# Kernel optimization log

Hardware: AMD Instinct MI355X
Metric: run time of the kernel (lower is better)

## Reference

```python
import jax, jax.numpy as jnp
import numpy as np


def _topk_gate(v, k):
    # keep values >= k-th largest (ties kept, matching torch semantics)
    topk_vals = jax.lax.top_k(v, k)[0]          # (B, k)
    thr = topk_vals[:, -1:]                      # (B, 1)
    return v * (v >= thr).astype(v.dtype)


def setup_inputs() -> dict:
    key = jax.random.key(0)
    ks = jax.random.split(key, 12)
    B, S, D, R, M = 8, 2048, 1024, 64, 256
    H = 4 * D
    def lin(k, fan_out, fan_in):
        bound = 1.0 / np.sqrt(fan_in)
        return jax.random.uniform(k, (fan_out, fan_in), jnp.float32, -bound, bound)
    def bias(k, fan_out, fan_in):
        bound = 1.0 / np.sqrt(fan_in)
        return jax.random.uniform(k, (fan_out,), jnp.float32, -bound, bound)
    return {
        "x": jax.random.normal(ks[0], (B, S, D), jnp.float32),
        "state": jnp.zeros((B, M), jnp.float32),
        "U_w": lin(ks[1], R, D),
        "V_w": lin(ks[2], R, D),
        "w1": lin(ks[3], H, D),
        "b1": bias(ks[4], H, D),
        "w2": lin(ks[5], D, H),
        "b2": bias(ks[6], D, H),
        "win_w": lin(ks[7], M, D),
        "win_b": bias(ks[8], M, D),
        "wstate": lin(ks[9], M, M),
        "gamma": jnp.float32(0.9),
        "top_k": 32,
    }


def reference(x, state, U_w, V_w, w1, b1, w2, b2, win_w, win_b, wstate, gamma, top_k):
    # outputs depend only on x (residual + FFN), computed vectorized over seq.
    h = jax.nn.relu(jnp.einsum("bsd,hd->bsh", x, w1) + b1)
    outputs = x + jnp.einsum("bsh,dh->bsd", h, w2) + b2   # (B, S, D)
    # Note: U_proj / V_proj are computed but unused in the original forward
    # (dead code); omitted here as they do not affect outputs or memory.

    # precompute W_in projection for all timesteps: (B, S, M)
    x_proj = jnp.einsum("bsd,md->bsm", x, win_w) + win_b

    def step(carry, xp_t):
        st, mem = carry
        su = jax.nn.relu(st @ wstate.T + xp_t)            # (B, M)
        g = _topk_gate(su, top_k)
        mem = gamma * mem + (1.0 - gamma) * g
        return (g, mem), None

    (_, memory), _ = jax.lax.scan(step, (state, state), jnp.swapaxes(x_proj, 0, 1))
    return outputs, memory
```

## Files before the change

kernel.cpp:

```cpp
#include <hip/hip_runtime.h>
#include <stdint.h>

#define BB 8
#define SS 2048
#define DD 1024
#define HH 4096
#define MM 256

typedef short bf16x8 __attribute__((ext_vector_type(8)));
typedef float f32x4 __attribute__((ext_vector_type(4)));

__device__ inline unsigned short f2bf(float f){
  unsigned u = __builtin_bit_cast(unsigned, f);
  return (unsigned short)((u + 0x7FFFu + ((u >> 16) & 1u)) >> 16);
}

__global__ void ssma_pack_bf16(const float* __restrict__ src,
                               unsigned short* __restrict__ dst, int n4){
  int i = blockIdx.x * blockDim.x + threadIdx.x;
  if (i < n4){
    float4 v = ((const float4*)src)[i];
    ushort4 o;
    o.x = f2bf(v.x); o.y = f2bf(v.y); o.z = f2bf(v.z); o.w = f2bf(v.w);
    ((ushort4*)dst)[i] = o;
  }
}

template<int EPI>
__global__ __launch_bounds__(256) void ssma_gemm_bt(
    const unsigned short* __restrict__ A, const unsigned short* __restrict__ Bw,
    int K, int N, const float* __restrict__ bias,
    const float* __restrict__ resid, void* __restrict__ Cout)
{
  __shared__ uint4 As4[512];
  __shared__ uint4 Bs4[512];
  unsigned short* As = (unsigned short*)As4;
  unsigned short* Bs = (unsigned short*)Bs4;

  const int tid  = threadIdx.x;
  const int lane = tid & 63;
  const int wv   = tid >> 6;
  const int wm   = wv >> 1, wn = wv & 1;
  const int m0   = blockIdx.y * 128;
  const int n0   = blockIdx.x * 128;
  const int kq   = lane >> 4;
  const int rl   = lane & 15;

  f32x4 acc[4][4];
#pragma unroll
  for (int a = 0; a < 4; ++a)
#pragma unroll
    for (int b = 0; b < 4; ++b) acc[a][b] = (f32x4){0.f, 0.f, 0.f, 0.f};

  for (int k0 = 0; k0 < K; k0 += 32){
    __syncthreads();
#pragma unroll
    for (int i = 0; i < 2; ++i){
      int c  = tid + 256 * i;
      int r  = c >> 2;
      int c8 = (c & 3) * 8;
      As4[c] = *(const uint4*)(A  + (size_t)(m0 + r) * K + k0 + c8);
      Bs4[c] = *(const uint4*)(Bw + (size_t)(n0 + r) * K + k0 + c8);
    }
    __syncthreads();

    const bf16x8* Ap = (const bf16x8*)As;
    const bf16x8* Bp = (const bf16x8*)Bs;
    bf16x8 af[4], bfr[4];
#pragma unroll
    for (int mi = 0; mi < 4; ++mi) af[mi]  = Ap[(wm * 64 + mi * 16 + rl) * 4 + kq];
#pragma unroll
    for (int ni = 0; ni < 4; ++ni) bfr[ni] = Bp[(wn * 64 + ni * 16 + rl) * 4 + kq];
#pragma unroll
    for (int mi = 0; mi < 4; ++mi)
#pragma unroll
      for (int ni = 0; ni < 4; ++ni)
        acc[mi][ni] = __builtin_amdgcn_mfma_f32_16x16x32_bf16(af[mi], bfr[ni], acc[mi][ni], 0, 0, 0);
  }

#pragma unroll
  for (int mi = 0; mi < 4; ++mi){
#pragma unroll
    for (int ni = 0; ni < 4; ++ni){
      int col = n0 + wn * 64 + ni * 16 + rl;
      float bv = bias[col];
#pragma unroll
      for (int r = 0; r < 4; ++r){
        int row = m0 + wm * 64 + mi * 16 + kq * 4 + r;
        float v = acc[mi][ni][r] + bv;
        if (EPI == 0){
          v = fmaxf(v, 0.0f);
          ((unsigned short*)Cout)[(size_t)row * N + col] = f2bf(v);
        } else {
          v += resid[(size_t)row * N + col];
          ((float*)Cout)[(size_t)row * N + col] = v;
        }
      }
    }
  }
}

__global__ __launch_bounds__(256) void ssma_gemm3_f32(
    const float* __restrict__ A, const float* __restrict__ Bw,
    const float* __restrict__ bias, float* __restrict__ C)
{
  __shared__ float As[64][17];
  __shared__ float Bs[64][17];
  const int tid = threadIdx.x;
  const int tx = tid & 15, ty = tid >> 4;
  const int m0 = blockIdx.y * 64, n0 = blockIdx.x * 64;
  float acc[4][4];
#pragma unroll
  for (int i = 0; i < 4; ++i)
#pragma unroll
    for (int j = 0; j < 4; ++j) acc[i][j] = 0.f;

  for (int k0 = 0; k0 < DD; k0 += 16){
    __syncthreads();
#pragma unroll
    for (int i = 0; i < 4; ++i){
      int e = tid + 256 * i;
      int r = e >> 4, c = e & 15;
      As[r][c] = A [(size_t)(m0 + r) * DD + k0 + c];
      Bs[r][c] = Bw[(size_t)(n0 + r) * DD + k0 + c];
    }
    __syncthreads();
#pragma unroll
    for (int kk = 0; kk < 16; ++kk){
      float a[4], b[4];
#pragma unroll
      for (int i = 0; i < 4; ++i) a[i] = As[ty * 4 + i][kk];
#pragma unroll
      for (int j = 0; j < 4; ++j) b[j] = Bs[tx * 4 + j][kk];
#pragma unroll
      for (int i = 0; i < 4; ++i)
#pragma unroll
        for (int j = 0; j < 4; ++j) acc[i][j] = fmaf(a[i], b[j], acc[i][j]);
    }
  }
#pragma unroll
  for (int i = 0; i < 4; ++i){
    int row = m0 + ty * 4 + i;
#pragma unroll
    for (int j = 0; j < 4; ++j){
      int col = n0 + tx * 4 + j;
      C[(size_t)row * MM + col] = acc[i][j] + bias[col];
    }
  }
}

__global__ __launch_bounds__(256) void ssma_transpose(
    const float* __restrict__ A, float* __restrict__ At)
{
  __shared__ float t[32][33];
  const int tx = threadIdx.x & 31, ty = threadIdx.x >> 5;
  const int x0 = blockIdx.x * 32, y0 = blockIdx.y * 32;
#pragma unroll
  for (int r = 0; r < 32; r += 8)
    t[ty + r][tx] = A[(size_t)(y0 + ty + r) * MM + x0 + tx];
  __syncthreads();
#pragma unroll
  for (int r = 0; r < 32; r += 8)
    At[(size_t)(x0 + ty + r) * MM + y0 + tx] = t[tx][ty + r];
}

__global__ __launch_bounds__(512) void ssma_scan2(
    const float* __restrict__ xproj, const float* __restrict__ state,
    const float* __restrict__ wT, const float* __restrict__ gamma_p,
    const int* __restrict__ topk_p, float* __restrict__ mem_out)
{
  __shared__ __align__(16) float su_all[MM];
  __shared__ __align__(16) float su_pos[MM + 32];
  __shared__ __align__(16) float val_list[MM + 8];
  __shared__ __align__(16) int   idx_list[MM + 8];
  __shared__ unsigned long long  umask[4];
  __shared__ unsigned int        kmask[8];

  const int tid  = threadIdx.x;
  const int wv   = tid >> 6;
  const int lane = tid & 63;
  const int b    = blockIdx.x;
  const float gamma = *gamma_p;
  const float omg   = 1.0f - gamma;
  const int   rk    = *topk_p - 1;

  const int m  = tid;
  const int hl = lane & 31;
  const int h  = lane >> 5;
  const int m2 = wv * 32 + hl;

  const float* xp  = xproj + (size_t)b * SS * MM;
  const float* wTm = wT + m;

  float mem = state[b * MM + m2];

  int nk_ch;
  float st0 = 0.0f;
  if (wv < 4){
    st0 = state[b * MM + m];
    unsigned long long pmi = __ballot(st0 != 0.0f);
    if (lane == 0) umask[wv] = pmi;
  }
  __syncthreads();
  {
    unsigned long long u0 = umask[0], u1 = umask[1], u2 = umask[2], u3 = umask[3];
    int nk = __popcll(u0) + __popcll(u1) + __popcll(u2) + __popcll(u3);
    if (wv < 4 && st0 != 0.0f){
      int before = (wv > 0 ? __popcll(u0) : 0) + (wv > 1 ? __popcll(u1) : 0)
                 + (wv > 2 ? __popcll(u2) : 0);
      unsigned long long pmw = (wv == 0 ? u0 : wv == 1 ? u1 : wv == 2 ? u2 : u3);
      int pos = before + __popcll(pmw & ((1ull << lane) - 1ull));
      idx_list[pos] = m << 8;
      val_list[pos] = st0;
    }
    if (tid < 8){ idx_list[nk + tid] = 0; val_list[nk + tid] = 0.0f; }
    nk_ch = (nk + 7) >> 3;
  }
  __syncthreads();

  float xp_cur = (wv < 4) ? xp[m] : 0.0f;

  for (int t = 0; t < SS; ++t){
    float su = 0.0f;
    unsigned long long pm = 0;
    float xp_next = 0.0f;
    if (wv < 4){
      int tn = (t + 1 < SS) ? t + 1 : SS - 1;
      xp_next = xp[(size_t)tn * MM + m];
      float s0=0.f,s1=0.f,s2=0.f,s3=0.f,s4=0.f,s5=0.f,s6=0.f,s7=0.f;
      const int4*   ipb = (const int4*)idx_list;
      const float4* vpb = (const float4*)val_list;
      for (int c = 0; c < nk_ch; ++c){
        int4   ia = ipb[2*c], ib = ipb[2*c+1];
        float4 va = vpb[2*c], vb = vpb[2*c+1];
        float w0 = wTm[ia.x], w1 = wTm[ia.y], w2 = wTm[ia.z], w3 = wTm[ia.w];
        float w4 = wTm[ib.x], w5 = wTm[ib.y], w6 = wTm[ib.z], w7 = wTm[ib.w];
        s0 = fmaf(w0, va.x, s0); s1 = fmaf(w1, va.y, s1);
        s2 = fmaf(w2, va.z, s2); s3 = fmaf(w3, va.w, s3);
        s4 = fmaf(w4, vb.x, s4); s5 = fmaf(w5, vb.y, s5);
        s6 = fmaf(w6, vb.z, s6); s7 = fmaf(w7, vb.w, s7);
      }
      float s = ((s0 + s1) + (s2 + s3)) + ((s4 + s5) + (s6 + s7));
      su = fmaxf(s + xp_cur, 0.0f);
      su_all[m] = su;
      pm = __ballot(su > 0.0f);
      if (lane == 0) umask[wv] = pm;
    }
    __syncthreads();

    int P;
    {
      unsigned long long u0 = umask[0], u1 = umask[1], u2 = umask[2], u3 = umask[3];
      P = __popcll(u0) + __popcll(u1) + __popcll(u2) + __popcll(u3);
      if (wv < 4 && su > 0.0f){
        int before = (wv > 0 ? __popcll(u0) : 0) + (wv > 1 ? __popcll(u1) : 0)
                   + (wv > 2 ? __popcll(u2) : 0);
        int pos = before + __popcll(pm & ((1ull << lane) - 1ull));
        su_pos[pos] = su;
      }
    }
    if (tid < 32) su_pos[P + tid] = 0.0f;
    __syncthreads();

    float su2 = su_all[m2];
    int CH16 = ((P + 31) >> 5) << 1;
    int half = CH16 >> 1;
    int base4 = h * half * 4;
    int cnt = 0;
    const float4* spp = (const float4*)su_pos;
    for (int c = 0; c < half; ++c){
      float4 a = spp[base4 + 4*c + 0];
      float4 q = spp[base4 + 4*c + 1];
      float4 r = spp[base4 + 4*c + 2];
      float4 d = spp[base4 + 4*c + 3];
      cnt += (a.x > su2) + (a.y > su2) + (a.z > su2) + (a.w > su2)
           + (q.x > su2) + (q.y > su2) + (q.z > su2) + (q.w > su2)
           + (r.x > su2) + (r.y > su2) + (r.z > su2) + (r.w > su2)
           + (d.x > su2) + (d.y > su2) + (d.z > su2) + (d.w > su2);
    }
    cnt += __shfl_xor(cnt, 32);
    float g = (su2 > 0.0f && cnt <= rk) ? su2 : 0.0f;
    if (h == 0) mem = fmaf(gamma, mem, omg * g);
    unsigned int km = (unsigned int)(__ballot(h == 0 && g > 0.0f) & 0xffffffffull);
    if (lane == 0) kmask[wv] = km;
    __syncthreads();

    {
      int nk = 0, before2 = 0;
#pragma unroll
      for (int wi = 0; wi < 8; ++wi){
        int pc = __popc(kmask[wi]);
        nk += pc;
        if (wi < wv) before2 += pc;
      }
      if (h == 0 && g > 0.0f){
        int pos2 = before2 + __popc(km & ((1u << hl) - 1u));
        idx_list[pos2] = m2 << 8;
        val_list[pos2] = g;
      }
      if (tid < 8){ idx_list[nk + tid] = 0; val_list[nk + tid] = 0.0f; }
      nk_ch = (nk + 7) >> 3;
    }
    xp_cur = xp_next;
    __syncthreads();
  }
  if (h == 0) mem_out[b * MM + m2] = mem;
}

extern "C" void kernel_launch(void* const* d_in, const int* in_sizes, int n_in,
                              void* d_out, int out_size, void* d_ws, size_t ws_size,
                              hipStream_t stream)
{
  const float* x      = (const float*)d_in[0];
  const float* state  = (const float*)d_in[1];
  const float* w1     = (const float*)d_in[4];
  const float* b1     = (const float*)d_in[5];
  const float* w2     = (const float*)d_in[6];
  const float* b2     = (const float*)d_in[7];
  const float* win_w  = (const float*)d_in[8];
  const float* win_b  = (const float*)d_in[9];
  const float* wstate = (const float*)d_in[10];
  const float* gammap = (const float*)d_in[11];
  const int*   topkp  = (const int*)d_in[12];

  float* out  = (float*)d_out;
  float* memo = out + (size_t)BB * SS * DD;

  char* ws = (char*)d_ws;
  unsigned short* xb   = (unsigned short*)(ws);
  unsigned short* w1b  = (unsigned short*)(ws + 33554432);
  unsigned short* w2b  = (unsigned short*)(ws + 41943040);
  unsigned short* hbuf = (unsigned short*)(ws + 50331648);
  float*          xprj = (float*)(ws + 184549376);
  float*          wT   = (float*)(ws + 33554432);

  ssma_pack_bf16<<<16384, 256, 0, stream>>>(x,  xb,  4194304);
  ssma_pack_bf16<<<4096,  256, 0, stream>>>(w1, w1b, 1048576);
  ssma_pack_bf16<<<4096,  256, 0, stream>>>(w2, w2b, 1048576);

  ssma_gemm3_f32<<<dim3(4, 256), 256, 0, stream>>>(x, win_w, win_b, xprj);

  ssma_gemm_bt<0><<<dim3(32, 128), 256, 0, stream>>>(xb, w1b, 1024, 4096, b1, nullptr, (void*)hbuf);

  ssma_transpose<<<dim3(8, 8), 256, 0, stream>>>(wstate, wT);

  ssma_gemm_bt<1><<<dim3(8, 128), 256, 0, stream>>>(hbuf, w2b, 4096, 1024, b2, x, (void*)out);

  ssma_scan2<<<BB, 512, 0, stream>>>(xprj, state, wT, gammap, topkp, memo);
}
```

Before: 5.781 ms.

## Rework scan kernel to 1024 threads with 4-way rank counting and unrolled gather

The sequential top-k scan kernel now runs 1024 threads per batch row instead of 512. Each of the 256 state elements gets four threads for the rank count, cutting per-thread comparison work, and the results are combined with two shuffles. The sparse matvec fully unrolls the first 32 active entries, since top_k=32 makes that the common case, and pads the list to multiples of 16. The cost is more barrier participants per step, wider block-level synchronization, and an extra loop for larger active sets.

```diff
diff --git a/kernel.cpp b/kernel.cpp
--- a/kernel.cpp
+++ b/kernel.cpp
@@ -164,17 +164,17 @@
     At[(size_t)(x0 + ty + r) * MM + y0 + tx] = t[tx][ty + r];
 }
 
-__global__ __launch_bounds__(512) void ssma_scan2(
+__global__ __launch_bounds__(1024) void ssma_scan4(
     const float* __restrict__ xproj, const float* __restrict__ state,
     const float* __restrict__ wT, const float* __restrict__ gamma_p,
     const int* __restrict__ topk_p, float* __restrict__ mem_out)
 {
   __shared__ __align__(16) float su_all[MM];
   __shared__ __align__(16) float su_pos[MM + 32];
-  __shared__ __align__(16) float val_list[MM + 8];
-  __shared__ __align__(16) int   idx_list[MM + 8];
-  __shared__ unsigned long long  umask[4];
-  __shared__ unsigned int        kmask[8];
+  __shared__ __align__(16) int   kidx[MM + 32];
+  __shared__ __align__(16) float kval[MM + 32];
+  __shared__ __align__(16) unsigned long long umask[4];
+  __shared__ __align__(16) int   kmask16[16];
 
   const int tid  = threadIdx.x;
   const int wv   = tid >> 6;
@@ -184,127 +184,156 @@
   const float omg   = 1.0f - gamma;
   const int   rk    = *topk_p - 1;
 
-  const int m  = tid;
-  const int hl = lane & 31;
-  const int h  = lane >> 5;
-  const int m2 = wv * 32 + hl;
+  const int r = tid >> 2;
+  const int q = tid & 3;
 
   const float* xp  = xproj + (size_t)b * SS * MM;
-  const float* wTm = wT + m;
-
-  float mem = state[b * MM + m2];
-
-  int nk_ch;
+  const float* wTm = wT + tid;
+
+  float mem = state[b * MM + r];
+
   float st0 = 0.0f;
-  if (wv < 4){
-    st0 = state[b * MM + m];
+  if (tid < MM){
+    st0 = state[b * MM + tid];
     unsigned long long pmi = __ballot(st0 != 0.0f);
     if (lane == 0) umask[wv] = pmi;
   }
   __syncthreads();
+  int nkp;
   {
     unsigned long long u0 = umask[0], u1 = umask[1], u2 = umask[2], u3 = umask[3];
     int nk = __popcll(u0) + __popcll(u1) + __popcll(u2) + __popcll(u3);
-    if (wv < 4 && st0 != 0.0f){
+    if (tid < MM && st0 != 0.0f){
       int before = (wv > 0 ? __popcll(u0) : 0) + (wv > 1 ? __popcll(u1) : 0)
                  + (wv > 2 ? __popcll(u2) : 0);
-      unsigned long long pmw = (wv == 0 ? u0 : wv == 1 ? u1 : wv == 2 ? u2 : u3);
-      int pos = before + __popcll(pmw & ((1ull << lane) - 1ull));
-      idx_list[pos] = m << 8;
-      val_list[pos] = st0;
-    }
-    if (tid < 8){ idx_list[nk + tid] = 0; val_list[nk + tid] = 0.0f; }
-    nk_ch = (nk + 7) >> 3;
-  }
+      unsigned long long mw = (wv == 0 ? u0 : wv == 1 ? u1 : wv == 2 ? u2 : u3);
+      int pos = before + __popcll(mw & ((1ull << lane) - 1ull));
+      kidx[pos] = tid << 8;
+      kval[pos] = st0;
+    }
+    nkp = (nk + 15) & ~15; if (nkp < 32) nkp = 32;
+    if (tid >= MM && tid < MM + 64){
+      int t2 = tid - MM;
+      if (nk + t2 < nkp){ kidx[nk + t2] = 0; kval[nk + t2] = 0.0f; }
+    }
+  }
+  float xp_cur = (tid < MM) ? xp[tid] : 0.0f;
   __syncthreads();
-
-  float xp_cur = (wv < 4) ? xp[m] : 0.0f;
 
   for (int t = 0; t < SS; ++t){
     float su = 0.0f;
-    unsigned long long pm = 0;
     float xp_next = 0.0f;
-    if (wv < 4){
+    if (tid < MM){
       int tn = (t + 1 < SS) ? t + 1 : SS - 1;
-      xp_next = xp[(size_t)tn * MM + m];
-      float s0=0.f,s1=0.f,s2=0.f,s3=0.f,s4=0.f,s5=0.f,s6=0.f,s7=0.f;
-      const int4*   ipb = (const int4*)idx_list;
-      const float4* vpb = (const float4*)val_list;
-      for (int c = 0; c < nk_ch; ++c){
-        int4   ia = ipb[2*c], ib = ipb[2*c+1];
-        float4 va = vpb[2*c], vb = vpb[2*c+1];
-        float w0 = wTm[ia.x], w1 = wTm[ia.y], w2 = wTm[ia.z], w3 = wTm[ia.w];
-        float w4 = wTm[ib.x], w5 = wTm[ib.y], w6 = wTm[ib.z], w7 = wTm[ib.w];
-        s0 = fmaf(w0, va.x, s0); s1 = fmaf(w1, va.y, s1);
-        s2 = fmaf(w2, va.z, s2); s3 = fmaf(w3, va.w, s3);
-        s4 = fmaf(w4, vb.x, s4); s5 = fmaf(w5, vb.y, s5);
-        s6 = fmaf(w6, vb.z, s6); s7 = fmaf(w7, vb.w, s7);
-      }
-      float s = ((s0 + s1) + (s2 + s3)) + ((s4 + s5) + (s6 + s7));
+      xp_next = xp[(size_t)tn * MM + tid];
+
+      const int4*   ip = (const int4*)kidx;
+      const float4* vp = (const float4*)kval;
+      float a0=0.f,a1=0.f,a2=0.f,a3=0.f,a4=0.f,a5=0.f,a6=0.f,a7=0.f;
+      {
+        int4 I0=ip[0], I1=ip[1], I2=ip[2], I3=ip[3];
+        float4 V0=vp[0], V1=vp[1], V2=vp[2], V3=vp[3];
+        float w00=wTm[I0.x], w01=wTm[I0.y], w02=wTm[I0.z], w03=wTm[I0.w];
+        float w10=wTm[I1.x], w11=wTm[I1.y], w12=wTm[I1.z], w13=wTm[I1.w];
+        float w20=wTm[I2.x], w21=wTm[I2.y], w22=wTm[I2.z], w23=wTm[I2.w];
+        float w30=wTm[I3.x], w31=wTm[I3.y], w32=wTm[I3.z], w33=wTm[I3.w];
+        a0=fmaf(w00,V0.x,a0); a1=fmaf(w01,V0.y,a1); a2=fmaf(w02,V0.z,a2); a3=fmaf(w03,V0.w,a3);
+        a4=fmaf(w10,V1.x,a4); a5=fmaf(w11,V1.y,a5); a6=fmaf(w12,V1.z,a6); a7=fmaf(w13,V1.w,a7);
+        a0=fmaf(w20,V2.x,a0); a1=fmaf(w21,V2.y,a1); a2=fmaf(w22,V2.z,a2); a3=fmaf(w23,V2.w,a3);
+        a4=fmaf(w30,V3.x,a4); a5=fmaf(w31,V3.y,a5); a6=fmaf(w32,V3.z,a6); a7=fmaf(w33,V3.w,a7);
+      }
+      {
+        int4 I0=ip[4], I1=ip[5], I2=ip[6], I3=ip[7];
+        float4 V0=vp[4], V1=vp[5], V2=vp[6], V3=vp[7];
+        float w00=wTm[I0.x], w01=wTm[I0.y], w02=wTm[I0.z], w03=wTm[I0.w];
+        float w10=wTm[I1.x], w11=wTm[I1.y], w12=wTm[I1.z], w13=wTm[I1.w];
+        float w20=wTm[I2.x], w21=wTm[I2.y], w22=wTm[I2.z], w23=wTm[I2.w];
+        float w30=wTm[I3.x], w31=wTm[I3.y], w32=wTm[I3.z], w33=wTm[I3.w];
+        a0=fmaf(w00,V0.x,a0); a1=fmaf(w01,V0.y,a1); a2=fmaf(w02,V0.z,a2); a3=fmaf(w03,V0.w,a3);
+        a4=fmaf(w10,V1.x,a4); a5=fmaf(w11,V1.y,a5); a6=fmaf(w12,V1.z,a6); a7=fmaf(w13,V1.w,a7);
+        a0=fmaf(w20,V2.x,a0); a1=fmaf(w21,V2.y,a1); a2=fmaf(w22,V2.z,a2); a3=fmaf(w23,V2.w,a3);
+        a4=fmaf(w30,V3.x,a4); a5=fmaf(w31,V3.y,a5); a6=fmaf(w32,V3.z,a6); a7=fmaf(w33,V3.w,a7);
+      }
+      if (nkp > 32){
+        for (int c4 = 8; c4 < (nkp >> 2); ++c4){
+          int4 I = ip[c4]; float4 V = vp[c4];
+          a0 = fmaf(wTm[I.x], V.x, a0); a1 = fmaf(wTm[I.y], V.y, a1);
+          a2 = fmaf(wTm[I.z], V.z, a2); a3 = fmaf(wTm[I.w], V.w, a3);
+        }
+      }
+      float s = ((a0 + a1) + (a2 + a3)) + ((a4 + a5) + (a6 + a7));
       su = fmaxf(s + xp_cur, 0.0f);
-      su_all[m] = su;
-      pm = __ballot(su > 0.0f);
+      su_all[tid] = su;
+      unsigned long long pm = __ballot(su > 0.0f);
       if (lane == 0) umask[wv] = pm;
     }
     __syncthreads();
 
-    int P;
+    int Ppad;
     {
       unsigned long long u0 = umask[0], u1 = umask[1], u2 = umask[2], u3 = umask[3];
-      P = __popcll(u0) + __popcll(u1) + __popcll(u2) + __popcll(u3);
-      if (wv < 4 && su > 0.0f){
+      int P = __popcll(u0) + __popcll(u1) + __popcll(u2) + __popcll(u3);
+      Ppad = (P + 15) & ~15;
+      if (tid < MM && su > 0.0f){
         int before = (wv > 0 ? __popcll(u0) : 0) + (wv > 1 ? __popcll(u1) : 0)
                    + (wv > 2 ? __popcll(u2) : 0);
-        int pos = before + __popcll(pm & ((1ull << lane) - 1ull));
+        unsigned long long mw = (wv == 0 ? u0 : wv == 1 ? u1 : wv == 2 ? u2 : u3);
+        int pos = before + __popcll(mw & ((1ull << lane) - 1ull));
         su_pos[pos] = su;
       }
-    }
-    if (tid < 32) su_pos[P + tid] = 0.0f;
-    __syncthreads();
-
-    float su2 = su_all[m2];
-    int CH16 = ((P + 31) >> 5) << 1;
-    int half = CH16 >> 1;
-    int base4 = h * half * 4;
+      if (tid >= MM && tid < MM + 32){
+        int t2 = tid - MM;
+        if (P + t2 < Ppad) su_pos[P + t2] = 0.0f;
+      }
+    }
+    __syncthreads();
+
+    float su2 = su_all[r];
+    int trips = Ppad >> 4;
     int cnt = 0;
     const float4* spp = (const float4*)su_pos;
-    for (int c = 0; c < half; ++c){
-      float4 a = spp[base4 + 4*c + 0];
-      float4 q = spp[base4 + 4*c + 1];
-      float4 r = spp[base4 + 4*c + 2];
-      float4 d = spp[base4 + 4*c + 3];
-      cnt += (a.x > su2) + (a.y > su2) + (a.z > su2) + (a.w > su2)
-           + (q.x > su2) + (q.y > su2) + (q.z > su2) + (q.w > su2)
-           + (r.x > su2) + (r.y > su2) + (r.z > su2) + (r.w > su2)
-           + (d.x > su2) + (d.y > su2) + (d.z > su2) + (d.w > su2);
-    }
-    cnt += __shfl_xor(cnt, 32);
+    for (int i = 0; i < trips; ++i){
+      float4 v = spp[i * 4 + q];
+      cnt += (v.x > su2) + (v.y > su2) + (v.z > su2) + (v.w > su2);
+    }
+    cnt += __shfl_xor(cnt, 1);
+    cnt += __shfl_xor(cnt, 2);
+
     float g = (su2 > 0.0f && cnt <= rk) ? su2 : 0.0f;
-    if (h == 0) mem = fmaf(gamma, mem, omg * g);
-    unsigned int km = (unsigned int)(__ballot(h == 0 && g > 0.0f) & 0xffffffffull);
-    if (lane == 0) kmask[wv] = km;
+    if (q == 0) mem = fmaf(gamma, mem, omg * g);
+
+    unsigned long long kb = __ballot(q == 0 && g > 0.0f);
+    unsigned long long kbS = kb & 0x1111111111111111ull;
+    if (lane == 0) kmask16[wv] = __popcll(kbS);
     __syncthreads();
 
     {
-      int nk = 0, before2 = 0;
-#pragma unroll
-      for (int wi = 0; wi < 8; ++wi){
-        int pc = __popc(kmask[wi]);
-        nk += pc;
-        if (wi < wv) before2 += pc;
-      }
-      if (h == 0 && g > 0.0f){
-        int pos2 = before2 + __popc(km & ((1u << hl) - 1u));
-        idx_list[pos2] = m2 << 8;
-        val_list[pos2] = g;
-      }
-      if (tid < 8){ idx_list[nk + tid] = 0; val_list[nk + tid] = 0.0f; }
-      nk_ch = (nk + 7) >> 3;
+      int4 k0 = *(const int4*)&kmask16[0];
+      int4 k1 = *(const int4*)&kmask16[4];
+      int4 k2 = *(const int4*)&kmask16[8];
+      int4 k3 = *(const int4*)&kmask16[12];
+      int cw[16] = {k0.x,k0.y,k0.z,k0.w, k1.x,k1.y,k1.z,k1.w,
+                    k2.x,k2.y,k2.z,k2.w, k3.x,k3.y,k3.z,k3.w};
+      int nk = 0, before = 0;
+#pragma unroll
+      for (int w = 0; w < 16; ++w){
+        nk += cw[w];
+        if (w < wv) before += cw[w];
+      }
+      if (q == 0 && g > 0.0f){
+        int pos = before + __popcll(kbS & ((1ull << lane) - 1ull));
+        kidx[pos] = r << 8;
+        kval[pos] = g;
+      }
+      nkp = (nk + 15) & ~15; if (nkp < 32) nkp = 32;
+      if (tid < 64){
+        if (nk + tid < nkp){ kidx[nk + tid] = 0; kval[nk + tid] = 0.0f; }
+      }
     }
     xp_cur = xp_next;
     __syncthreads();
   }
-  if (h == 0) mem_out[b * MM + m2] = mem;
+  if (q == 0) mem_out[b * MM + r] = mem;
 }
 
 extern "C" void kernel_launch(void* const* d_in, const int* in_sizes, int n_in,
@@ -346,5 +375,5 @@
 
   ssma_gemm_bt<1><<<dim3(8, 128), 256, 0, stream>>>(hbuf, w2b, 4096, 1024, b2, x, (void*)out);
 
-  ssma_scan2<<<BB, 512, 0, stream>>>(xprj, state, wT, gammap, topkp, memo);
-}
+  ssma_scan4<<<BB, 1024, 0, stream>>>(xprj, state, wT, gammap, topkp, memo);
+}
```

After: 5.448 ms. -5.8%, faster.
